# Performance work log

Hardware: AMD Instinct MI355X
Metric: run time of the kernel (lower is better)

## Reference

```python
import jax, jax.numpy as jnp
import numpy as np

GRID = 16
PAD = 32
RADIUS = 8
SIGMA = 1.5
B = 8192
N_SEEDS = 24


def setup_inputs() -> dict:
    key = jax.random.key(0)
    k1, k2 = jax.random.split(key)
    # predicted seeds: (x, y, phase), coords in [0, GRID)
    output = jax.random.uniform(k1, (B, N_SEEDS * 3), dtype=jnp.float32) * GRID
    # target seeds: (x, y, amp), coords in [0, 2*GRID)
    targets = jax.random.uniform(k2, (B, N_SEEDS * 3), dtype=jnp.float32) * (2 * GRID)
    return {"output": output, "targets": targets}


def _forward(output, targets):
    Bn = output.shape[0]
    seeds = output.reshape(Bn, -1, 3)   # (B, N, 3): x, y, phase
    tgt = targets.reshape(Bn, -1, 3)    # (B, M, 3): x, y, amp

    # --- discrete Voronoi on GRID x GRID (vectorized over batch) ---
    c = jnp.arange(GRID, dtype=output.dtype)
    xx, yy = jnp.meshgrid(c, c, indexing='ij')  # (GRID, GRID)
    dist = jnp.sqrt((xx[None, :, :, None] - seeds[:, None, None, :, 0]) ** 2
                    + (yy[None, :, :, None] - seeds[:, None, None, :, 1]) ** 2)
    labels = jnp.argmin(dist, axis=-1)  # (B, GRID, GRID) int

    # circular support on the inner grid (np.ogrid[-r:r, -r:r] convention)
    cc = jnp.arange(-RADIUS, RADIUS)
    inner = (cc[:, None] ** 2 + cc[None, :] ** 2) <= RADIUS ** 2
    labels = jnp.where(inner[None], labels, 0)

    # zero-pad voronoi labels to PAD x PAD
    pw = (PAD - GRID) // 2
    padded = jnp.pad(labels, ((0, 0), (pw, pw), (pw, pw)))  # (B, PAD, PAD)

    # --- gather phase per pixel, zero outside circle on padded grid ---
    phases = seeds[:, :, 2]  # (B, N)
    phase = jnp.take_along_axis(phases, padded.reshape(Bn, -1), axis=1).reshape(Bn, PAD, PAD)
    pc = jnp.arange(PAD)
    center = PAD // 2
    outside = (pc[:, None] - center) ** 2 + (pc[None, :] - center) ** 2 > RADIUS ** 2
    phase = jnp.where(outside[None], jnp.zeros_like(phase), phase)

    # --- density = amp(=1) * exp(i * 2*pi * phase), shifted FFT magnitude ---
    two_pi = 2.0 * jnp.pi
    density = jax.lax.complex(jnp.cos(two_pi * phase), jnp.sin(two_pi * phase))
    pred = jnp.fft.fftshift(density, axes=(-2, -1))
    pred = jnp.fft.fft2(pred)
    pred_dp = jnp.abs(jnp.fft.fftshift(pred, axes=(-2, -1)))  # (B, PAD, PAD)

    # --- target diffraction: sum of Gaussians on (2*GRID)x(2*GRID) grid ---
    xc = jnp.arange(PAD, dtype=targets.dtype)  # height == width == 2*GRID == PAD
    tx = tgt[:, :, 0][:, :, None, None]
    ty = tgt[:, :, 1][:, :, None, None]
    amp = tgt[:, :, 2][:, :, None, None]
    # torch: x varies along last axis, y along second-to-last
    d2 = (xc[None, None, None, :] - tx) ** 2 + (xc[None, None, :, None] - ty) ** 2
    tgt_dp = jnp.sum(amp * jnp.exp(-d2 / (2.0 * SIGMA ** 2)), axis=1)  # (B, PAD, PAD)

    # --- chi-square (global max-normalization and reductions) ---
    p = pred_dp / jnp.max(pred_dp)
    t = tgt_dp / jnp.max(tgt_dp)
    return jnp.sum((p - t) ** 2) / jnp.sqrt(jnp.sum(p ** 2) * jnp.sum(t ** 2))


def reference(output, targets):
    return _forward(output, targets)
```

## Files before the change

kernel.cpp:

```cpp
#include <hip/hip_runtime.h>
#include <math.h>

#define NS 24

typedef float v2f __attribute__((ext_vector_type(2)));
typedef float v4f __attribute__((ext_vector_type(4)));


struct PixTab { unsigned short v[196]; };
__device__ constexpr PixTab make_pix() {
    PixTab t{};
    int n = 0;
    const int w[16] = {0,3,5,6,6,7,7,7,8,7,7,7,6,6,5,3};
    for (int yy = 0; yy < 16; ++yy)
        for (int x = 16 - w[yy]; x <= 16 + w[yy]; ++x)
            if (x < 24) { t.v[n] = (unsigned short)((yy << 8) | x); n = n + 1; }
    t.v[195] = (unsigned short)((8 << 8) | 24);
    return t;
}
__device__ constexpr PixTab PIX = make_pix();

struct ZTab { unsigned short v[76]; };
__device__ constexpr ZTab make_ztab() {
    ZTab z{};
    bool mark[16][17] = {};
    const int w[16] = {0,3,5,6,6,7,7,7,8,7,7,7,6,6,5,3};
    for (int yy = 0; yy < 16; ++yy)
        for (int x = 16 - w[yy]; x <= 16 + w[yy]; ++x)
            if (x < 24) mark[yy][x - 8] = true;
    mark[8][16] = true;
    int n = 0;
    for (int yy = 0; yy < 16; ++yy)
        for (int xi = 0; xi < 17; ++xi)
            if (!mark[yy][xi]) { z.v[n] = (unsigned short)(yy * 18 + xi); n = n + 1; }
    return z;
}
__device__ constexpr ZTab ZT = make_ztab();

constexpr float twc_(int p) {
    const float C[17] = {
        1.0f, 0.98078528040323044913f, 0.92387953251128675613f, 0.83146961230254523708f,
        0.70710678118654752440f, 0.55557023301960222474f, 0.38268343236508977173f,
        0.19509032201612826785f, 0.0f,
        -0.19509032201612826785f, -0.38268343236508977173f, -0.55557023301960222474f,
        -0.70710678118654752440f, -0.83146961230254523708f, -0.92387953251128675613f,
        -0.98078528040323044913f, -1.0f };
    return (p <= 16) ? C[p] : C[32 - p];
}
constexpr float tws_(int p) {
    const float S[17] = {
        0.0f, 0.19509032201612826785f, 0.38268343236508977173f, 0.55557023301960222474f,
        0.70710678118654752440f, 0.83146961230254523708f, 0.92387953251128675613f,
        0.98078528040323044913f, 1.0f,
        0.98078528040323044913f, 0.92387953251128675613f, 0.83146961230254523708f,
        0.70710678118654752440f, 0.55557023301960222474f, 0.38268343236508977173f,
        0.19509032201612826785f, 0.0f };
    return (p <= 16) ? -S[p] : S[32 - p];
}
struct alignas(16) TW1T { float v[8 * 18 * 2]; };
__device__ constexpr TW1T make_tw1() {
    TW1T t{};
    for (int l0 = 0; l0 < 8; ++l0)
        for (int xi = 0; xi < 17; ++xi) {
            int p = (l0 * (xi + 8)) & 31;
            t.v[(l0 * 18 + xi) * 2 + 0] = twc_(p);
            t.v[(l0 * 18 + xi) * 2 + 1] = tws_(p);
        }
    return t;
}
__device__ constexpr TW1T TW1G = make_tw1();
struct alignas(16) TW2T { float v[4 * 18 * 2]; };
__device__ constexpr TW2T make_tw2() {
    TW2T t{};
    for (int k0 = 0; k0 < 4; ++k0)
        for (int yp = 0; yp < 16; ++yp) {
            int p = (k0 * (yp + 8)) & 31;
            t.v[(k0 * 18 + yp) * 2 + 0] = twc_(p);
            t.v[(k0 * 18 + yp) * 2 + 1] = tws_(p);
        }
    return t;
}
__device__ constexpr TW2T TW2G = make_tw2();

static __device__ __forceinline__ v2f cmul(v2f e, v2f w) {
    v2f m = (v2f){e.y, e.y} * (v2f){w.y, w.x};
    return __builtin_elementwise_fma((v2f){e.x, e.x}, w, (v2f){-m.x, m.y});
}
static __device__ __forceinline__ float mag(v2f h) {
    v2f q = h * h;
    return sqrtf(q.x + q.y);
}

template <int CTRL>
static __device__ __forceinline__ float dpp_step(float x) {
    int y = __builtin_amdgcn_update_dpp(0, __float_as_int(x), CTRL, 0xf, 0xf, true);
    return __int_as_float(y);
}
static __device__ __forceinline__ float wave_sum(float x) {
    x += dpp_step<0x111>(x);
    x += dpp_step<0x112>(x);
    x += dpp_step<0x114>(x);
    x += dpp_step<0x118>(x);
    x += dpp_step<0x142>(x);
    x += dpp_step<0x143>(x);
    return x;
}
static __device__ __forceinline__ float wave_max(float x) {
    x = fmaxf(x, dpp_step<0x111>(x));
    x = fmaxf(x, dpp_step<0x112>(x));
    x = fmaxf(x, dpp_step<0x114>(x));
    x = fmaxf(x, dpp_step<0x118>(x));
    x = fmaxf(x, dpp_step<0x142>(x));
    x = fmaxf(x, dpp_step<0x143>(x));
    return x;
}

__global__ __launch_bounds__(256)
void loss_main(const float* __restrict__ output, const float* __restrict__ targets,
               float* __restrict__ partials, int B) {
    __shared__ float2 e24s;
    __shared__ __align__(16) float gx[NS * 32];
    __shared__ __align__(16) float gyT[32 * 24];
    __shared__ __align__(16) float e2f[16 * 18 * 2];
    __shared__ __align__(16) float tw2f[4 * 36];
    __shared__ __align__(16) float gT2f[32 * 36];
    __shared__ __align__(16) char uA[5120];

    float* tw1f = (float*)uA;
    float* pmf  = (float*)uA;

    const int b = blockIdx.x;
    const int t = threadIdx.x;
    const float* so = output + b * NS * 3;
    const float* tg = targets + b * NS * 3;

    if (t == 0) {
        float sv0, cv0;
        __sincosf(6.2831853071795864f * so[2], &sv0, &cv0);
        e24s = make_float2(cv0 - 1.0f, sv0);
    }
    if (t < 108) {
        if (t < 72) *(v4f*)&tw1f[t * 4] = *(const v4f*)&TW1G.v[t * 4];
        else        *(v4f*)&tw2f[(t - 72) * 4] = *(const v4f*)&TW2G.v[(t - 72) * 4];
    }
    for (int idx = t; idx < NS * 32; idx += 256) {
        int s = idx >> 5, c = idx & 31;
        float dx = (float)c - tg[3 * s];
        gx[idx] = tg[3 * s + 2] * __expf(dx * dx * (-1.0f / 4.5f));
    }
    for (int idx = t; idx < 32 * 24; idx += 256) {
        int r = idx / 24, s = idx - r * 24;
        float dy = (float)r - tg[3 * s + 1];
        gyT[idx] = __expf(dy * dy * (-1.0f / 4.5f));
    }
    if (t < 98) {
        int pv0 = PIX.v[t], pv1 = PIX.v[t + 98];
        int yy0 = pv0 >> 8, x0 = (pv0 & 255) - 8;
        int yy1 = pv1 >> 8, x1 = (pv1 & 255) - 8;
        v2f FI = {(float)yy0, (float)yy1};
        v2f FJ = {(float)x0, (float)x1};
        v2f bd = {1e30f, 1e30f};
        v2f bph = {0.f, 0.f};
#pragma unroll
        for (int s = 0; s < NS; ++s) {
            float sx = so[3 * s], sy = so[3 * s + 1], phs = so[3 * s + 2];
            v2f dX = FI - (v2f){sx, sx};
            v2f dY = FJ - (v2f){sy, sy};
            v2f d2 = __builtin_elementwise_fma(dX, dX, dY * dY);
            if (d2.x < bd.x) { bd.x = d2.x; bph.x = phs; }
            if (d2.y < bd.y) { bd.y = d2.y; bph.y = phs; }
        }
        float ph1 = (t == 97) ? so[2] : bph.y;
        float sv0, cv0, sv1, cv1;
        __sincosf(6.2831853071795864f * bph.x, &sv0, &cv0);
        __sincosf(6.2831853071795864f * ph1, &sv1, &cv1);
        *(v2f*)&e2f[(yy0 * 18 + x0) * 2] = (v2f){cv0 - 1.0f, sv0};
        *(v2f*)&e2f[(yy1 * 18 + x1) * 2] = (v2f){cv1 - 1.0f, sv1};
    } else if (t < 98 + 76) {
        int idx = (int)ZT.v[t - 98];
        *(v2f*)&e2f[idx * 2] = (v2f){0.f, 0.f};
    }
    __syncthreads();

    if (t < 128) {
        int yy = t >> 3, l0 = t & 7;
        const float* row = &e2f[yy * 36];
        const float* twr = &tw1f[l0 * 36];
        v2f c0 = {0,0}, c1 = {0,0}, c2 = {0,0}, c3 = {0,0};
#pragma unroll
        for (int q = 0; q < 8; ++q) {
            v4f e4 = *(const v4f*)&row[q * 4];
            v4f w4 = *(const v4f*)&twr[q * 4];
            v2f ca = cmul((v2f){e4.x, e4.y}, (v2f){w4.x, w4.y});
            v2f cb = cmul((v2f){e4.z, e4.w}, (v2f){w4.z, w4.w});
            if ((q & 1) == 0) { c0 += ca; c1 += cb; }
            else              { c2 += ca; c3 += cb; }
        }
        {
            v2f e16 = *(const v2f*)&row[32];
            v2f w16 = *(const v2f*)&twr[32];
            c0 += cmul(e16, w16);
        }
        v2f a = c0 + c2, bb = c0 - c2;
        v2f cc = c1 + c3, d = c1 - c3;
        v2f du = {d.y, -d.x};
        *(v2f*)&gT2f[l0 * 36 + yy * 2]        = a + cc;
        *(v2f*)&gT2f[(l0 + 8) * 36 + yy * 2]  = bb + du;
        *(v2f*)&gT2f[(l0 + 16) * 36 + yy * 2] = a - cc;
        *(v2f*)&gT2f[(l0 + 24) * 36 + yy * 2] = bb - du;
    }
    __syncthreads();

    if (t < 128) {
        int l = t >> 2, k0 = t & 3;
        const float* gTr = &gT2f[l * 36];
        const float* twr = &tw2f[k0 * 36];
        v2f c[8];
#pragma unroll
        for (int q = 0; q < 4; ++q) {
            v4f glo = *(const v4f*)&gTr[q * 4];
            v4f ghi = *(const v4f*)&gTr[q * 4 + 16];
            v4f wlo = *(const v4f*)&twr[q * 4];
            v4f whi = *(const v4f*)&twr[q * 4 + 16];
            c[2 * q]     = cmul((v2f){glo.x, glo.y}, (v2f){wlo.x, wlo.y})
                         + cmul((v2f){ghi.x, ghi.y}, (v2f){whi.x, whi.y});
            c[2 * q + 1] = cmul((v2f){glo.z, glo.w}, (v2f){wlo.z, wlo.w})
                         + cmul((v2f){ghi.z, ghi.w}, (v2f){whi.z, whi.w});
        }
        v2f Ea = c[0] + c[4], Eb = c[0] - c[4];
        v2f Ec = c[2] + c[6], Ed = c[2] - c[6];
        v2f Edu = {Ed.y, -Ed.x};
        v2f E0 = Ea + Ec, E1 = Eb + Edu, E2 = Ea - Ec, E3 = Eb - Edu;
        v2f Oa = c[1] + c[5], Ob = c[1] - c[5];
        v2f Oc = c[3] + c[7], Od = c[3] - c[7];
        v2f Odu = {Od.y, -Od.x};
        v2f O0 = Oa + Oc, O1 = Ob + Odu, O2 = Oa - Oc, O3 = Ob - Odu;
        const float s2 = 0.70710678118654752440f;
        v2f w1O = (v2f){s2, s2} * (v2f){O1.x + O1.y, O1.y - O1.x};
        v2f w3O = (v2f){s2, s2} * (v2f){O3.y - O3.x, -(O3.x + O3.y)};
        v2f miO = {O2.y, -O2.x};
        {
            float2 e24 = e24s;
            float ar2 = (k0 == 0) ? 1.f : (k0 == 2) ? -1.f : 0.f;
            float ai2 = (k0 == 1) ? 1.f : (k0 == 3) ? -1.f : 0.f;
            float sgn = (l & 1) ? -1.f : 1.f;
            v2f T = {sgn * (e24.x * ar2 - e24.y * ai2),
                     sgn * (e24.x * ai2 + e24.y * ar2)};
            E0 += T; E1 += T; E2 += T; E3 += T;
        }
        v2f h0 = E0 + O0;
        if (t == 0) h0.x += 1024.0f;
        int v = (l + 16) & 31;
        pmf[(k0 + 16) * 40 + v] = mag(h0);
        pmf[(k0 + 20) * 40 + v] = mag(E1 + w1O);
        pmf[(k0 + 24) * 40 + v] = mag(E2 + miO);
        pmf[(k0 + 28) * 40 + v] = mag(E3 + w3O);
        pmf[(k0)      * 40 + v] = mag(E0 - O0);
        pmf[(k0 + 4)  * 40 + v] = mag(E1 - w1O);
        pmf[(k0 + 8)  * 40 + v] = mag(E2 - miO);
        pmf[(k0 + 12) * 40 + v] = mag(E3 - w3O);
    }
    __syncthreads();

    if (t < 64) {
        int rr = t >> 3;
        int c0i = (t & 7) * 4;
        v2f a01[4] = {{0,0},{0,0},{0,0},{0,0}};
        v2f a23[4] = {{0,0},{0,0},{0,0},{0,0}};
#pragma unroll
        for (int q = 0; q < 6; ++q) {
            v4f gy0 = *(const v4f*)&gyT[rr * 24 + q * 4];
            v4f gy1 = *(const v4f*)&gyT[(rr + 8) * 24 + q * 4];
            v4f gy2 = *(const v4f*)&gyT[(rr + 16) * 24 + q * 4];
            v4f gy3 = *(const v4f*)&gyT[(rr + 24) * 24 + q * 4];
#pragma unroll
            for (int j = 0; j < 4; ++j) {
                v4f g4 = *(const v4f*)&gx[(4 * q + j) * 32 + c0i];
                float g0 = (j == 0) ? gy0.x : (j == 1) ? gy0.y : (j == 2) ? gy0.z : gy0.w;
                float g1 = (j == 0) ? gy1.x : (j == 1) ? gy1.y : (j == 2) ? gy1.z : gy1.w;
                float g2 = (j == 0) ? gy2.x : (j == 1) ? gy2.y : (j == 2) ? gy2.z : gy2.w;
                float g3 = (j == 0) ? gy3.x : (j == 1) ? gy3.y : (j == 2) ? gy3.z : gy3.w;
                v2f glo = {g4.x, g4.y}, ghi = {g4.z, g4.w};
                a01[0] = __builtin_elementwise_fma((v2f){g0, g0}, glo, a01[0]);
                a23[0] = __builtin_elementwise_fma((v2f){g0, g0}, ghi, a23[0]);
                a01[1] = __builtin_elementwise_fma((v2f){g1, g1}, glo, a01[1]);
                a23[1] = __builtin_elementwise_fma((v2f){g1, g1}, ghi, a23[1]);
                a01[2] = __builtin_elementwise_fma((v2f){g2, g2}, glo, a01[2]);
                a23[2] = __builtin_elementwise_fma((v2f){g2, g2}, ghi, a23[2]);
                a01[3] = __builtin_elementwise_fma((v2f){g3, g3}, glo, a01[3]);
                a23[3] = __builtin_elementwise_fma((v2f){g3, g3}, ghi, a23[3]);
            }
        }
        float sp2 = 0.f, st2 = 0.f, spt = 0.f, mp = 0.f, mt = 0.f;
#pragma unroll
        for (int k = 0; k < 4; ++k) {
            v4f p4 = *(const v4f*)&pmf[(rr + 8 * k) * 40 + c0i];
            v2f p01 = {p4.x, p4.y}, p23 = {p4.z, p4.w};
            v2f s2v = __builtin_elementwise_fma(p23, p23, p01 * p01);
            v2f t2v = __builtin_elementwise_fma(a23[k], a23[k], a01[k] * a01[k]);
            v2f ptv = __builtin_elementwise_fma(p23, a23[k], p01 * a01[k]);
            sp2 += s2v.x + s2v.y;
            st2 += t2v.x + t2v.y;
            spt += ptv.x + ptv.y;
            mp = fmaxf(mp, fmaxf(fmaxf(p4.x, p4.y), fmaxf(p4.z, p4.w)));
            v2f tm = __builtin_elementwise_max(a01[k], a23[k]);
            mt = fmaxf(mt, fmaxf(tm.x, tm.y));
        }
        sp2 = wave_sum(sp2);
        st2 = wave_sum(st2);
        spt = wave_sum(spt);
        mp  = wave_max(mp);
        mt  = wave_max(mt);
        if (t == 63) {
            partials[0 * B + b] = sp2;
            partials[1 * B + b] = st2;
            partials[2 * B + b] = spt;
            partials[3 * B + b] = mp;
            partials[4 * B + b] = mt;
        }
    }
}

__global__ __launch_bounds__(1024)
void finalize_loss(const float* __restrict__ partials, float* __restrict__ out, int B) {
    __shared__ double reds[16][3];
    __shared__ float redx[16][2];
    const int t = threadIdx.x;
    double sp2 = 0.0, st2 = 0.0, spt = 0.0;
    float mp = 0.f, mt = 0.f;
    for (int i = t; i < B; i += 1024) {
        sp2 += (double)partials[0 * B + i];
        st2 += (double)partials[1 * B + i];
        spt += (double)partials[2 * B + i];
        mp = fmaxf(mp, partials[3 * B + i]);
        mt = fmaxf(mt, partials[4 * B + i]);
    }
    for (int off = 32; off > 0; off >>= 1) {
        sp2 += __shfl_down(sp2, off);
        st2 += __shfl_down(st2, off);
        spt += __shfl_down(spt, off);
        mp = fmaxf(mp, __shfl_down(mp, off));
        mt = fmaxf(mt, __shfl_down(mt, off));
    }
    int wave = t >> 6, lane = t & 63;
    if (lane == 0) {
        reds[wave][0] = sp2; reds[wave][1] = st2; reds[wave][2] = spt;
        redx[wave][0] = mp;  redx[wave][1] = mt;
    }
    __syncthreads();
    if (t == 0) {
        for (int w = 1; w < 16; ++w) {
            sp2 += reds[w][0];
            st2 += reds[w][1];
            spt += reds[w][2];
            mp = fmaxf(mp, redx[w][0]);
            mt = fmaxf(mt, redx[w][1]);
        }
        double Mp = (double)mp, Mt = (double)mt;
        double loss = (sp2 * (Mt / Mp) + st2 * (Mp / Mt) - 2.0 * spt) / sqrt(sp2 * st2);
        out[0] = (float)loss;
    }
}

extern "C" void kernel_launch(void* const* d_in, const int* in_sizes, int n_in,
                              void* d_out, int out_size, void* d_ws, size_t ws_size,
                              hipStream_t stream) {
    const float* output  = (const float*)d_in[0];
    const float* targets = (const float*)d_in[1];
    int B = in_sizes[0] / (NS * 3);
    float* partials = (float*)d_ws;

    loss_main<<<B, 256, 0, stream>>>(output, targets, partials, B);
    finalize_loss<<<1, 1024, 0, stream>>>(partials, (float*)d_out, B);
}
```

Measured before the change: 97.81 us.

## Overlap target Gaussian matmul with FFT stage on idle waves

Moves the separable Gaussian target computation from a single wave at the end onto the otherwise idle threads 128-255 during the first FFT pass, keeping the results in registers. The final reduction is then spread over two waves and combined through a small shared-memory array plus an extra barrier. This shortens the serial tail of the kernel but adds a sync and raises register pressure on the upper waves.

```diff
diff --git a/kernel.cpp b/kernel.cpp
--- a/kernel.cpp
+++ b/kernel.cpp
@@ -125,6 +125,7 @@
     __shared__ __align__(16) float tw2f[4 * 36];
     __shared__ __align__(16) float gT2f[32 * 36];
     __shared__ __align__(16) char uA[5120];
+    __shared__ float redm[2][5];
 
     float* tw1f = (float*)uA;
     float* pmf  = (float*)uA;
@@ -182,6 +183,8 @@
     }
     __syncthreads();
 
+    v2f ta01 = {0,0}, ta23 = {0,0}, tb01 = {0,0}, tb23 = {0,0};
+
     if (t < 128) {
         int yy = t >> 3, l0 = t & 7;
         const float* row = &e2f[yy * 36];
@@ -208,6 +211,26 @@
         *(v2f*)&gT2f[(l0 + 8) * 36 + yy * 2]  = bb + du;
         *(v2f*)&gT2f[(l0 + 16) * 36 + yy * 2] = a - cc;
         *(v2f*)&gT2f[(l0 + 24) * 36 + yy * 2] = bb - du;
+    } else {
+        int tid2 = t - 128;
+        int r = tid2 >> 3;
+        int c0i = (tid2 & 7) * 4;
+#pragma unroll
+        for (int q = 0; q < 6; ++q) {
+            v4f gy4a = *(const v4f*)&gyT[r * 24 + q * 4];
+            v4f gy4b = *(const v4f*)&gyT[(r + 16) * 24 + q * 4];
+#pragma unroll
+            for (int j = 0; j < 4; ++j) {
+                v4f g4 = *(const v4f*)&gx[(4 * q + j) * 32 + c0i];
+                float ga = (j == 0) ? gy4a.x : (j == 1) ? gy4a.y : (j == 2) ? gy4a.z : gy4a.w;
+                float gb = (j == 0) ? gy4b.x : (j == 1) ? gy4b.y : (j == 2) ? gy4b.z : gy4b.w;
+                v2f glo = {g4.x, g4.y}, ghi = {g4.z, g4.w};
+                ta01 = __builtin_elementwise_fma((v2f){ga, ga}, glo, ta01);
+                ta23 = __builtin_elementwise_fma((v2f){ga, ga}, ghi, ta23);
+                tb01 = __builtin_elementwise_fma((v2f){gb, gb}, glo, tb01);
+                tb23 = __builtin_elementwise_fma((v2f){gb, gb}, ghi, tb23);
+            }
+        }
     }
     __syncthreads();
 
@@ -262,62 +285,43 @@
     }
     __syncthreads();
 
-    if (t < 64) {
-        int rr = t >> 3;
-        int c0i = (t & 7) * 4;
-        v2f a01[4] = {{0,0},{0,0},{0,0},{0,0}};
-        v2f a23[4] = {{0,0},{0,0},{0,0},{0,0}};
-#pragma unroll
-        for (int q = 0; q < 6; ++q) {
-            v4f gy0 = *(const v4f*)&gyT[rr * 24 + q * 4];
-            v4f gy1 = *(const v4f*)&gyT[(rr + 8) * 24 + q * 4];
-            v4f gy2 = *(const v4f*)&gyT[(rr + 16) * 24 + q * 4];
-            v4f gy3 = *(const v4f*)&gyT[(rr + 24) * 24 + q * 4];
-#pragma unroll
-            for (int j = 0; j < 4; ++j) {
-                v4f g4 = *(const v4f*)&gx[(4 * q + j) * 32 + c0i];
-                float g0 = (j == 0) ? gy0.x : (j == 1) ? gy0.y : (j == 2) ? gy0.z : gy0.w;
-                float g1 = (j == 0) ? gy1.x : (j == 1) ? gy1.y : (j == 2) ? gy1.z : gy1.w;
-                float g2 = (j == 0) ? gy2.x : (j == 1) ? gy2.y : (j == 2) ? gy2.z : gy2.w;
-                float g3 = (j == 0) ? gy3.x : (j == 1) ? gy3.y : (j == 2) ? gy3.z : gy3.w;
-                v2f glo = {g4.x, g4.y}, ghi = {g4.z, g4.w};
-                a01[0] = __builtin_elementwise_fma((v2f){g0, g0}, glo, a01[0]);
-                a23[0] = __builtin_elementwise_fma((v2f){g0, g0}, ghi, a23[0]);
-                a01[1] = __builtin_elementwise_fma((v2f){g1, g1}, glo, a01[1]);
-                a23[1] = __builtin_elementwise_fma((v2f){g1, g1}, ghi, a23[1]);
-                a01[2] = __builtin_elementwise_fma((v2f){g2, g2}, glo, a01[2]);
-                a23[2] = __builtin_elementwise_fma((v2f){g2, g2}, ghi, a23[2]);
-                a01[3] = __builtin_elementwise_fma((v2f){g3, g3}, glo, a01[3]);
-                a23[3] = __builtin_elementwise_fma((v2f){g3, g3}, ghi, a23[3]);
-            }
-        }
-        float sp2 = 0.f, st2 = 0.f, spt = 0.f, mp = 0.f, mt = 0.f;
-#pragma unroll
-        for (int k = 0; k < 4; ++k) {
-            v4f p4 = *(const v4f*)&pmf[(rr + 8 * k) * 40 + c0i];
-            v2f p01 = {p4.x, p4.y}, p23 = {p4.z, p4.w};
-            v2f s2v = __builtin_elementwise_fma(p23, p23, p01 * p01);
-            v2f t2v = __builtin_elementwise_fma(a23[k], a23[k], a01[k] * a01[k]);
-            v2f ptv = __builtin_elementwise_fma(p23, a23[k], p01 * a01[k]);
-            sp2 += s2v.x + s2v.y;
-            st2 += t2v.x + t2v.y;
-            spt += ptv.x + ptv.y;
-            mp = fmaxf(mp, fmaxf(fmaxf(p4.x, p4.y), fmaxf(p4.z, p4.w)));
-            v2f tm = __builtin_elementwise_max(a01[k], a23[k]);
-            mt = fmaxf(mt, fmaxf(tm.x, tm.y));
-        }
+    if (t >= 128) {
+        int tid2 = t - 128;
+        int r = tid2 >> 3;
+        int c0i = (tid2 & 7) * 4;
+        v4f p4a = *(const v4f*)&pmf[r * 40 + c0i];
+        v4f p4b = *(const v4f*)&pmf[(r + 16) * 40 + c0i];
+        v2f pa01 = {p4a.x, p4a.y}, pa23 = {p4a.z, p4a.w};
+        v2f pb01 = {p4b.x, p4b.y}, pb23 = {p4b.z, p4b.w};
+        v2f s2v = pa01 * pa01 + pa23 * pa23 + pb01 * pb01 + pb23 * pb23;
+        v2f t2v = ta01 * ta01 + ta23 * ta23 + tb01 * tb01 + tb23 * tb23;
+        v2f ptv = pa01 * ta01 + pa23 * ta23 + pb01 * tb01 + pb23 * tb23;
+        float sp2 = s2v.x + s2v.y;
+        float st2 = t2v.x + t2v.y;
+        float spt = ptv.x + ptv.y;
+        float mp = fmaxf(fmaxf(fmaxf(p4a.x, p4a.y), fmaxf(p4a.z, p4a.w)),
+                         fmaxf(fmaxf(p4b.x, p4b.y), fmaxf(p4b.z, p4b.w)));
+        v2f tm = __builtin_elementwise_max(__builtin_elementwise_max(ta01, ta23),
+                                           __builtin_elementwise_max(tb01, tb23));
+        float mt = fmaxf(tm.x, tm.y);
         sp2 = wave_sum(sp2);
         st2 = wave_sum(st2);
         spt = wave_sum(spt);
         mp  = wave_max(mp);
         mt  = wave_max(mt);
-        if (t == 63) {
-            partials[0 * B + b] = sp2;
-            partials[1 * B + b] = st2;
-            partials[2 * B + b] = spt;
-            partials[3 * B + b] = mp;
-            partials[4 * B + b] = mt;
-        }
+        int wv = (t >> 6) - 2, lane = t & 63;
+        if (lane == 63) {
+            redm[wv][0] = sp2; redm[wv][1] = st2; redm[wv][2] = spt;
+            redm[wv][3] = mp;  redm[wv][4] = mt;
+        }
+    }
+    __syncthreads();
+    if (t == 0) {
+        partials[0 * B + b] = redm[0][0] + redm[1][0];
+        partials[1 * B + b] = redm[0][1] + redm[1][1];
+        partials[2 * B + b] = redm[0][2] + redm[1][2];
+        partials[3 * B + b] = fmaxf(redm[0][3], redm[1][3]);
+        partials[4 * B + b] = fmaxf(redm[0][4], redm[1][4]);
     }
 }
 
```

New measurement: 95.28 us (median of 2 runs). 1.03x faster.
